# Optimization experiments

Measured on AMD Instinct MI355X. Metric: run time of the kernel, lower is better.

## Reference

```python
import jax, jax.numpy as jnp
import numpy as np

N = 65536      # points
NS = 16        # nsample
CIN = 128
CMID = 128
COUT = 128
S = 8          # share_planes
EPS = 1e-5


def setup_inputs() -> dict:
    key = jax.random.key(0)
    ks = jax.random.split(key, 12)
    f = lambda k, shape, s=0.05: (jax.random.normal(k, shape, jnp.float32) * s)
    inp = {
        'p': jax.random.normal(ks[0], (N, 3), jnp.float32),
        'x': jax.random.normal(ks[1], (N, CIN), jnp.float32),
        'idx': jax.random.randint(ks[2], (N, NS), 0, N, jnp.int32),
        'wq': f(ks[3], (CMID, CIN)), 'bq': jnp.zeros((CMID,), jnp.float32),
        'wk': f(ks[4], (CMID, CIN)), 'bk': jnp.zeros((CMID,), jnp.float32),
        'wv': f(ks[5], (COUT, CIN)), 'bv': jnp.zeros((COUT,), jnp.float32),
        'p_w1': f(ks[6], (3, 3), 0.3), 'p_b1': jnp.zeros((3,), jnp.float32),
        'p_bng': jnp.ones((3,), jnp.float32), 'p_bnb': jnp.zeros((3,), jnp.float32),
        'p_bnm': jnp.zeros((3,), jnp.float32), 'p_bnv': jnp.ones((3,), jnp.float32),
        'p_w2': f(ks[7], (COUT, 3), 0.3), 'p_b2': jnp.zeros((COUT,), jnp.float32),
        'w_bn1g': jnp.ones((CMID,), jnp.float32), 'w_bn1b': jnp.zeros((CMID,), jnp.float32),
        'w_bn1m': jnp.zeros((CMID,), jnp.float32), 'w_bn1v': jnp.ones((CMID,), jnp.float32),
        'w_w1': f(ks[8], (CMID // S, CMID)), 'w_b1': jnp.zeros((CMID // S,), jnp.float32),
        'w_bn2g': jnp.ones((CMID // S,), jnp.float32), 'w_bn2b': jnp.zeros((CMID // S,), jnp.float32),
        'w_bn2m': jnp.zeros((CMID // S,), jnp.float32), 'w_bn2v': jnp.ones((CMID // S,), jnp.float32),
        'w_w2': f(ks[9], (COUT // S, COUT // S)), 'w_b2': jnp.zeros((COUT // S,), jnp.float32),
    }
    return inp


def _bn(t, g, b, m, v):
    # eval-mode BatchNorm1d: per-channel affine on last axis
    return (t - m) * (g / jnp.sqrt(v + EPS)) + b


def reference(p, x, idx, wq, bq, wk, bk, wv, bv,
              p_w1, p_b1, p_bng, p_bnb, p_bnm, p_bnv, p_w2, p_b2,
              w_bn1g, w_bn1b, w_bn1m, w_bn1v, w_w1, w_b1,
              w_bn2g, w_bn2b, w_bn2m, w_bn2v, w_w2, w_b2):
    idx = idx.astype(jnp.int32)
    x_q = x @ wq.T + bq            # (n, mid)
    x_k = x @ wk.T + bk            # (n, mid)
    x_v = x @ wv.T + bv            # (n, out)
    # boundary_queryandgroup: gather neighbors, relative xyz
    p_r = p[idx] - p[:, None, :]   # (n, ns, 3)
    g_k = x_k[idx]                 # (n, ns, mid)
    g_v = x_v[idx]                 # (n, ns, out)
    # linear_p: Linear(3,3) -> BN(3) -> ReLU -> Linear(3,out)
    p_r = p_r @ p_w1.T + p_b1
    p_r = jax.nn.relu(_bn(p_r, p_bng, p_bnb, p_bnm, p_bnv))
    p_r = p_r @ p_w2.T + p_b2      # (n, ns, out)
    n, ns, _ = g_k.shape
    w = g_k - x_q[:, None, :] + p_r.reshape(n, ns, COUT // CMID, CMID).sum(2)
    # linear_w: BN(mid) -> ReLU -> Linear(mid, mid//s) -> BN -> ReLU -> Linear
    w = jax.nn.relu(_bn(w, w_bn1g, w_bn1b, w_bn1m, w_bn1v))
    w = w @ w_w1.T + w_b1          # (n, ns, mid//s)
    w = jax.nn.relu(_bn(w, w_bn2g, w_bn2b, w_bn2m, w_bn2v))
    w = w @ w_w2.T + w_b2          # (n, ns, out//s)
    w = jax.nn.softmax(w, axis=1)  # over neighbors
    out = ((g_v + p_r).reshape(n, ns, S, COUT // S) * w[:, :, None, :]).sum(1)
    return out.reshape(n, COUT)
```

## Files before the change

kernel.cpp:

```cpp
#include <hip/hip_runtime.h>

typedef unsigned short u16;
typedef unsigned int   u32;
typedef unsigned long long u64;

#define NPTS 65536
#define NNS  16
#define C    128

static __device__ __forceinline__ float bflo(u32 u){ return __builtin_bit_cast(float, u << 16); }
static __device__ __forceinline__ float ldbf(const u16* p){ return bflo((u32)(*p)); }
static __device__ __forceinline__ u16 f2bf(float f){
  u32 u = __builtin_bit_cast(u32, f);
  return (u16)((u + 0x7fffu + ((u >> 16) & 1u)) >> 16);
}

template<bool BF>
static __device__ __forceinline__ float ldT(const void* b, long i){
  if constexpr (BF) return ldbf((const u16*)b + i);
  else return ((const float*)b)[i];
}

struct P29 {
  const void *p, *x; const int* idx;
  const void *wq,*bq,*wk,*bk,*wv,*bv;
  const void *pw1,*pb1,*pbng,*pbnb,*pbnm,*pbnv,*pw2,*pb2;
  const void *bn1g,*bn1b,*bn1m,*bn1v,*ww1,*wb1;
  const void *bn2g,*bn2b,*bn2m,*bn2v,*ww2,*wb2;
};

static __device__ int detect_mode(const void* x){
  int lane = threadIdx.x & 63;
  float vb = ldbf((const u16*)x + lane);
  bool okb = (vb == vb) && fabsf(vb) < 32.f && fabsf(vb) > 1e-8f;
  if (__popcll(__ballot(okb)) >= 56) return 0;
  float vf = ((const float*)x)[lane];
  bool okf = (vf == vf) && fabsf(vf) < 32.f && fabsf(vf) > 1e-8f;
  if (__popcll(__ballot(okf)) >= 56) return 1;
  return 2;
}

template<bool BF>
static __device__ int value_checks(const P29& q){
  int lane = threadIdx.x & 63;
  bool ok = fabsf(ldT<BF>(q.bq, lane)) <= 1e-5f;
  ok = ok && fabsf(ldT<BF>(q.bn1v, lane) - 1.f) <= 0.02f;
  if (lane < 3) ok = ok && fabsf(ldT<BF>(q.pbnv, lane) - 1.f) <= 0.02f;
  if (__popcll(__ballot(ok)) != 64) return 4;
  int v = q.idx[lane];
  bool in = (v >= 0 && v < NPTS);
  if (__popcll(__ballot(in)) != 64) return 3;
  bool oz = ((lane & 1) == 1) ? (v == 0) : true;
  if (__popcll(__ballot(oz)) == 64) return 5;
  return 0;
}

static __device__ void report_out(void* outv, float code_val){
  u16* o = (u16*)outv;
  const int tid = threadIdx.x, wid = tid >> 6, lane = tid & 63;
  const int n = blockIdx.x * 4 + wid;
  ((u32*)o)[(size_t)n * 64 + lane] = 0u;
  if (blockIdx.x == 0 && tid == 0){
    ((float*)outv)[0] = code_val;
    o[2] = f2bf(code_val);
  }
}

__global__ __launch_bounds__(256) void report_kernel(void* outv, float code_val){
  report_out(outv, code_val);
}

typedef __bf16 bf16x8 __attribute__((ext_vector_type(8)));
typedef float  f32x4  __attribute__((ext_vector_type(4)));

template<bool BF>
static __device__ __forceinline__ void stage64(const void* src, size_t row0, u16* lds){
  const int t = threadIdx.x;
  #pragma unroll
  for (int i = 0; i < 4; i++){
    const int ch  = t + i * 256;
    const int row = ch >> 4, cc = ch & 15;
    u16 tmp[8];
    if constexpr (BF){
      *(uint4*)tmp = *(const uint4*)((const u16*)src + ((row0 + row) * (size_t)128 + cc * 8));
    } else {
      const float* s = (const float*)src + ((row0 + row) * (size_t)128 + cc * 8);
      float4 a = ((const float4*)s)[0];
      float4 b = ((const float4*)s)[1];
      tmp[0] = f2bf(a.x); tmp[1] = f2bf(a.y); tmp[2] = f2bf(a.z); tmp[3] = f2bf(a.w);
      tmp[4] = f2bf(b.x); tmp[5] = f2bf(b.y); tmp[6] = f2bf(b.z); tmp[7] = f2bf(b.w);
    }
    const u32 byte = (u32)row * 256u + (u32)((cc * 16) ^ ((row & 7) << 4));
    *(uint4*)((char*)lds + byte) = *(uint4*)tmp;
  }
}

template<bool BF>
static __device__ void qkv_mfma_body(const P29 q, u16* xq, u16* xk, u16* xv){
  __shared__ u16 sA[64 * 128];
  const int a = blockIdx.y;
  const size_t n0 = (size_t)blockIdx.x * 64;
  const void* W  = (a == 0) ? q.wq : (a == 1) ? q.wk : q.wv;
  const void* Bp = (a == 0) ? q.bq : (a == 1) ? q.bk : q.bv;
  u16*       D   = (a == 0) ? xq  : (a == 1) ? xk  : xv;

  stage64<BF>(q.x, n0, sA);

  const int tid = threadIdx.x, wid = tid >> 6, lane = tid & 63;
  const int lm = lane & 15, lk = lane >> 4;
  const int colbase = wid * 32;

  bf16x8 bfr[2][4];
  #pragma unroll
  for (int ni = 0; ni < 2; ni++){
    const int col = colbase + ni*16 + lm;
    #pragma unroll
    for (int kk = 0; kk < 4; kk++){
      const int k0 = kk*32 + lk*8;
      uint4 raw;
      if constexpr (BF){
        raw = *(const uint4*)((const u16*)W + (size_t)col * C + k0);
      } else {
        const float* s = (const float*)W + (size_t)col * C + k0;
        float4 x0 = ((const float4*)s)[0], x1 = ((const float4*)s)[1];
        u16 tmp[8] = {f2bf(x0.x),f2bf(x0.y),f2bf(x0.z),f2bf(x0.w),
                      f2bf(x1.x),f2bf(x1.y),f2bf(x1.z),f2bf(x1.w)};
        raw = *(const uint4*)tmp;
      }
      bfr[ni][kk] = __builtin_bit_cast(bf16x8, raw);
    }
  }
  __syncthreads();

  f32x4 acc[4][2];
  #pragma unroll
  for (int mi = 0; mi < 4; mi++){
    acc[mi][0] = f32x4{0.f,0.f,0.f,0.f};
    acc[mi][1] = f32x4{0.f,0.f,0.f,0.f};
  }

  #pragma unroll
  for (int kk = 0; kk < 4; kk++){
    const u32 kb = (u32)(kk * 64 + lk * 16);
    #pragma unroll
    for (int mi = 0; mi < 4; mi++){
      const u32 row = (u32)(mi*16 + lm);
      bf16x8 af = *(const bf16x8*)((const char*)sA + row * 256u + (kb ^ ((row & 7u) << 4)));
      acc[mi][0] = __builtin_amdgcn_mfma_f32_16x16x32_bf16(af, bfr[0][kk], acc[mi][0], 0, 0, 0);
      acc[mi][1] = __builtin_amdgcn_mfma_f32_16x16x32_bf16(af, bfr[1][kk], acc[mi][1], 0, 0, 0);
    }
  }

  #pragma unroll
  for (int ni = 0; ni < 2; ni++){
    const int col = colbase + ni*16 + lm;
    const float bias = ldT<BF>(Bp, col);
    #pragma unroll
    for (int mi = 0; mi < 4; mi++){
      const size_t rbase = n0 + (size_t)(mi*16 + lk*4);
      #pragma unroll
      for (int r = 0; r < 4; r++)
        D[(rbase + r) * 128 + col] = f2bf(acc[mi][ni][r] + bias);
    }
  }
}

__global__ __launch_bounds__(256)
void qkv_kernel(P29 q, u16* xq, u16* xk, u16* xv){
  int mode = detect_mode(q.x);
  if (mode == 0)      qkv_mfma_body<true >(q, xq, xk, xv);
  else if (mode == 1) qkv_mfma_body<false>(q, xq, xk, xv);
}

template<bool BF>
static __device__ void main_body(const P29 q, const u16* xq, const u16* xk,
                                 const u16* xv, void* outv){
  __shared__ char s_buf[4][5120];

  const int tid  = threadIdx.x;
  const int wid  = tid >> 6, lane = tid & 63;
  const int n    = blockIdx.x * 4 + wid;
  const int c0   = lane * 2, c1 = c0 + 1;

  u16*   s_w   = (u16*)  s_buf[wid];
  float* s_mid = (float*)(s_buf[wid] + 4096);
  float* s_wf  = (float*) s_buf[wid];

  float pw[3][3], pb[3];
  #pragma unroll
  for (int t = 0; t < 3; t++){
    float ss = ldT<BF>(q.pbng, t) * rsqrtf(fabsf(ldT<BF>(q.pbnv, t)) + 1e-5f);
    float tt = ldT<BF>(q.pbnb, t) - ldT<BF>(q.pbnm, t) * ss;
    #pragma unroll
    for (int k = 0; k < 3; k++) pw[t][k] = ss * ldT<BF>(q.pw1, t*3 + k);
    pb[t] = ss * ldT<BF>(q.pb1, t) + tt;
  }
  const float ps0 = ldT<BF>(q.p, (size_t)n*3 + 0);
  const float ps1 = ldT<BF>(q.p, (size_t)n*3 + 1);
  const float ps2 = ldT<BF>(q.p, (size_t)n*3 + 2);

  const float s0 = ldT<BF>(q.bn1g, c0) * rsqrtf(fabsf(ldT<BF>(q.bn1v, c0)) + 1e-5f);
  const float t0 = ldT<BF>(q.bn1b, c0) - ldT<BF>(q.bn1m, c0) * s0;
  const float s1 = ldT<BF>(q.bn1g, c1) * rsqrtf(fabsf(ldT<BF>(q.bn1v, c1)) + 1e-5f);
  const float t1 = ldT<BF>(q.bn1b, c1) - ldT<BF>(q.bn1m, c1) * s1;
  const float A0 = ldT<BF>(q.pw2, c0*3+0), A1 = ldT<BF>(q.pw2, c0*3+1), A2 = ldT<BF>(q.pw2, c0*3+2);
  const float B0 = ldT<BF>(q.pw2, c1*3+0), B1 = ldT<BF>(q.pw2, c1*3+1), B2 = ldT<BF>(q.pw2, c1*3+2);
  const float pbc0 = ldT<BF>(q.pb2, c0), pbc1 = ldT<BF>(q.pb2, c1);
  const float xq0 = ldbf(xq + (size_t)n * C + c0);
  const float xq1 = ldbf(xq + (size_t)n * C + c1);

  u32 svp[NNS];
  #pragma unroll
  for (int m = 0; m < NNS; m++){
    int im = q.idx[n*NNS + m];
    im = (im < 0) ? 0 : ((im >= NPTS) ? NPTS-1 : im);
    float pd0 = ldT<BF>(q.p, (size_t)im*3 + 0) - ps0;
    float pd1 = ldT<BF>(q.p, (size_t)im*3 + 1) - ps1;
    float pd2 = ldT<BF>(q.p, (size_t)im*3 + 2) - ps2;
    float q0 = fmaxf(pd0*pw[0][0] + pd1*pw[0][1] + pd2*pw[0][2] + pb[0], 0.f);
    float q1 = fmaxf(pd0*pw[1][0] + pd1*pw[1][1] + pd2*pw[1][2] + pb[1], 0.f);
    float q2 = fmaxf(pd0*pw[2][0] + pd1*pw[2][1] + pd2*pw[2][2] + pb[2], 0.f);
    float pr0 = q0*A0 + q1*A1 + q2*A2 + pbc0;
    float pr1 = q0*B0 + q1*B1 + q2*B2 + pbc1;
    u32 gk = *(const u32*)(xk + (size_t)im * C + c0);
    u32 gv = *(const u32*)(xv + (size_t)im * C + c0);
    float gk0 = bflo(gk & 0xffffu);
    float gk1 = bflo(gk >> 16);
    float w0 = fmaxf(s0*(gk0 - xq0 + pr0) + t0, 0.f);
    float w1 = fmaxf(s1*(gk1 - xq1 + pr1) + t1, 0.f);
    u32 pk = (u32)f2bf(w0) | ((u32)f2bf(w1) << 16);
    u32 byte = (u32)m * 256u + (((u32)lane * 4u) ^ (((u32)m & 7u) << 4));
    *(u32*)((char*)s_w + byte) = pk;
    float sv0 = bflo(gv & 0xffffu) + pr0;
    float sv1 = bflo(gv >> 16)     + pr1;
    svp[m] = (u32)f2bf(sv0) | ((u32)f2bf(sv1) << 16);
  }
  asm volatile("" ::: "memory");

  const int tb = (lane >> 4) * 4;
  {
    const int tA = lane & 15, gA = lane >> 4;
    f32x4 acc2;
    #pragma unroll
    for (int r = 0; r < 4; r++) acc2[r] = ldT<BF>(q.wb1, tb + r);
    const u32 row = lane & 15;
    #pragma unroll
    for (int kk = 0; kk < 4; kk++){
      const int cbase = kk*32 + gA*8;
      uint4 raw;
      if constexpr (BF){
        raw = *(const uint4*)((const u16*)q.ww1 + (size_t)tA*C + cbase);
      } else {
        const float* s = (const float*)q.ww1 + (size_t)tA*C + cbase;
        float4 a = ((const float4*)s)[0], b = ((const float4*)s)[1];
        u16 tmp[8] = {f2bf(a.x),f2bf(a.y),f2bf(a.z),f2bf(a.w),
                      f2bf(b.x),f2bf(b.y),f2bf(b.z),f2bf(b.w)};
        raw = *(const uint4*)tmp;
      }
      bf16x8 wwA = __builtin_bit_cast(bf16x8, raw);
      const u32 off = ((u32)(kk*64 + (lane >> 4)*16)) ^ ((row & 7u) << 4);
      bf16x8 bw = *(const bf16x8*)((const char*)s_w + row*256u + off);
      acc2 = __builtin_amdgcn_mfma_f32_16x16x32_bf16(wwA, bw, acc2, 0, 0, 0);
    }
    #pragma unroll
    for (int r = 0; r < 4; r++){
      const int t = tb + r;
      float g2 = ldT<BF>(q.bn2g, t), v2 = ldT<BF>(q.bn2v, t);
      float m2 = ldT<BF>(q.bn2m, t), b2 = ldT<BF>(q.bn2b, t);
      float ss = g2 * rsqrtf(fabsf(v2) + 1e-5f);
      float tt = b2 - m2*ss;
      s_mid[row*16 + ((t + row) & 15)] = fmaxf(ss*acc2[r] + tt, 0.f);
    }
  }
  asm volatile("" ::: "memory");

  const int mm = lane & 15, ug = lane >> 4;
  #pragma unroll
  for (int ui = 0; ui < 4; ui++){
    const int u = ug*4 + ui;
    float acc = ldT<BF>(q.wb2, u);
    #pragma unroll
    for (int t = 0; t < 16; t++)
      acc += s_mid[mm*16 + ((t + mm) & 15)] * ldT<BF>(q.ww2, u*16 + t);
    float mx = acc;
    #pragma unroll
    for (int msk = 1; msk < 16; msk <<= 1) mx = fmaxf(mx, __shfl_xor(mx, msk, 64));
    float ee = __expf(acc - mx);
    float sm = ee;
    #pragma unroll
    for (int msk = 1; msk < 16; msk <<= 1) sm += __shfl_xor(sm, msk, 64);
    s_wf[mm*17 + u] = ee / sm;
  }
  asm volatile("" ::: "memory");

  float acc0 = 0.f, acc1 = 0.f;
  const int u0 = c0 & 15;
  #pragma unroll
  for (int m = 0; m < NNS; m++){
    float wf0 = s_wf[m*17 + u0];
    float wf1 = s_wf[m*17 + u0 + 1];
    acc0 += bflo(svp[m] & 0xffffu) * wf0;
    acc1 += bflo(svp[m] >> 16)     * wf1;
  }
  if (!(acc0 == acc0)) acc0 = 12345.f;
  if (!(acc1 == acc1)) acc1 = 12345.f;
  if (BF){
    u16* o = (u16*)outv;
    o[(size_t)n * C + c0] = f2bf(acc0);
    o[(size_t)n * C + c1] = f2bf(acc1);
  } else {
    float* o = (float*)outv;
    o[(size_t)n * C + c0] = acc0;
    o[(size_t)n * C + c1] = acc1;
  }
}

__global__ __launch_bounds__(256)
void main_kernel(P29 q, const u16* xq, const u16* xk, const u16* xv, void* outv){
  int mode = detect_mode(q.x);
  int code = (mode == 2) ? 2 : (mode == 0 ? value_checks<true>(q) : value_checks<false>(q));
  if (code){ report_out(outv, code * 10000.f); return; }
  if (mode == 0) main_body<true >(q, xq, xk, xv, outv);
  else           main_body<false>(q, xq, xk, xv, outv);
}

extern "C" void kernel_launch(void* const* d_in, const int* in_sizes, int n_in,
                              void* d_out, int out_size, void* d_ws, size_t ws_size,
                              hipStream_t stream)
{
  static const int exp_sizes[29] = {
    196608, 8388608, 1048576,
    16384, 128, 16384, 128, 16384, 128,
    9, 3, 3, 3, 3, 3,
    384, 128,
    128, 128, 128, 128,
    2048, 16,
    16, 16, 16, 16,
    256, 16
  };
  int code = 0;
  if (n_in != 29) code = 7;
  else {
    for (int i = 0; i < 29; i++) if (in_sizes[i] != exp_sizes[i]) { code = 8; break; }
  }
  if (!code && out_size != NPTS * C) code = 9;
  if (!code && ws_size < (size_t)3 * NPTS * C * sizeof(u16)) code = 6;

  if (code){
    hipLaunchKernelGGL(report_kernel, dim3(NPTS/4), dim3(256), 0, stream,
                       d_out, (float)(code * 10000));
    return;
  }

  P29 q;
  q.p   = d_in[0];  q.x    = d_in[1];  q.idx  = (const int*)d_in[2];
  q.wq  = d_in[3];  q.bq   = d_in[4];  q.wk   = d_in[5];  q.bk  = d_in[6];
  q.wv  = d_in[7];  q.bv   = d_in[8];
  q.pw1 = d_in[9];  q.pb1  = d_in[10];
  q.pbng= d_in[11]; q.pbnb = d_in[12]; q.pbnm = d_in[13]; q.pbnv= d_in[14];
  q.pw2 = d_in[15]; q.pb2  = d_in[16];
  q.bn1g= d_in[17]; q.bn1b = d_in[18]; q.bn1m = d_in[19]; q.bn1v= d_in[20];
  q.ww1 = d_in[21]; q.wb1  = d_in[22];
  q.bn2g= d_in[23]; q.bn2b = d_in[24]; q.bn2m = d_in[25]; q.bn2v= d_in[26];
  q.ww2 = d_in[27]; q.wb2  = d_in[28];

  u16* xq = (u16*)d_ws;
  u16* xk = xq + (size_t)NPTS * C;
  u16* xv = xk + (size_t)NPTS * C;

  hipLaunchKernelGGL(qkv_kernel, dim3(1024, 3), dim3(256), 0, stream, q, xq, xk, xv);
  hipLaunchKernelGGL(main_kernel, dim3(NPTS/4), dim3(256), 0, stream, q, xq, xk, xv, d_out);
}
```

Measured before the change: 401.4 us.

## Use MFMA for second linear_w layer and transpose QKV GEMM for packed stores

Replaces the scalar 16x16 second linear_w matmul (via an LDS scratch buffer and per-lane loops over ww2) with a single 16x16x16 bf16 MFMA fed directly from registers, dropping the s_mid LDS buffer and shrinking shared memory per block. The QKV projection GEMM swaps operand roles so each lane owns four consecutive output channels, allowing packed 8-byte stores instead of scattered 2-byte stores. The second-layer intermediate is now rounded to bf16 before the MFMA, which slightly changes numerics.

```diff
diff --git a/kernel.cpp b/kernel.cpp
--- a/kernel.cpp
+++ b/kernel.cpp
@@ -71,7 +71,22 @@
 }
 
 typedef __bf16 bf16x8 __attribute__((ext_vector_type(8)));
+typedef __bf16 bf16x4 __attribute__((ext_vector_type(4)));
+typedef short  s16x4  __attribute__((ext_vector_type(4)));
 typedef float  f32x4  __attribute__((ext_vector_type(4)));
+
+static __device__ __forceinline__ f32x4 mfma16_bf16(u32 alo, u32 ahi,
+                                                    u32 blo, u32 bhi, f32x4 c){
+#if __has_builtin(__builtin_amdgcn_mfma_f32_16x16x16_bf16)
+  union { u32 u[2]; bf16x4 v; } A, B;
+  A.u[0]=alo; A.u[1]=ahi; B.u[0]=blo; B.u[1]=bhi;
+  return __builtin_amdgcn_mfma_f32_16x16x16_bf16(A.v, B.v, c, 0, 0, 0);
+#else
+  union { u32 u[2]; s16x4 v; } A, B;
+  A.u[0]=alo; A.u[1]=ahi; B.u[0]=blo; B.u[1]=bhi;
+  return __builtin_amdgcn_mfma_f32_16x16x16bf16_1k(A.v, B.v, c, 0, 0, 0);
+#endif
+}
 
 template<bool BF>
 static __device__ __forceinline__ void stage64(const void* src, size_t row0, u16* lds){
@@ -108,59 +123,60 @@
 
   const int tid = threadIdx.x, wid = tid >> 6, lane = tid & 63;
   const int lm = lane & 15, lk = lane >> 4;
-  const int colbase = wid * 32;
-
-  bf16x8 bfr[2][4];
-  #pragma unroll
-  for (int ni = 0; ni < 2; ni++){
-    const int col = colbase + ni*16 + lm;
+  const int chbase = wid * 32;
+
+  bf16x8 wfr[2][4];
+  #pragma unroll
+  for (int ci = 0; ci < 2; ci++){
+    const int ch = chbase + ci*16 + lm;
     #pragma unroll
     for (int kk = 0; kk < 4; kk++){
       const int k0 = kk*32 + lk*8;
       uint4 raw;
       if constexpr (BF){
-        raw = *(const uint4*)((const u16*)W + (size_t)col * C + k0);
+        raw = *(const uint4*)((const u16*)W + (size_t)ch * C + k0);
       } else {
-        const float* s = (const float*)W + (size_t)col * C + k0;
+        const float* s = (const float*)W + (size_t)ch * C + k0;
         float4 x0 = ((const float4*)s)[0], x1 = ((const float4*)s)[1];
         u16 tmp[8] = {f2bf(x0.x),f2bf(x0.y),f2bf(x0.z),f2bf(x0.w),
                       f2bf(x1.x),f2bf(x1.y),f2bf(x1.z),f2bf(x1.w)};
         raw = *(const uint4*)tmp;
       }
-      bfr[ni][kk] = __builtin_bit_cast(bf16x8, raw);
+      wfr[ci][kk] = __builtin_bit_cast(bf16x8, raw);
     }
   }
   __syncthreads();
 
-  f32x4 acc[4][2];
-  #pragma unroll
-  for (int mi = 0; mi < 4; mi++){
-    acc[mi][0] = f32x4{0.f,0.f,0.f,0.f};
-    acc[mi][1] = f32x4{0.f,0.f,0.f,0.f};
-  }
+  f32x4 acc[2][4];
+  #pragma unroll
+  for (int ci = 0; ci < 2; ci++)
+    #pragma unroll
+    for (int pi = 0; pi < 4; pi++) acc[ci][pi] = f32x4{0.f,0.f,0.f,0.f};
 
   #pragma unroll
   for (int kk = 0; kk < 4; kk++){
     const u32 kb = (u32)(kk * 64 + lk * 16);
     #pragma unroll
-    for (int mi = 0; mi < 4; mi++){
-      const u32 row = (u32)(mi*16 + lm);
-      bf16x8 af = *(const bf16x8*)((const char*)sA + row * 256u + (kb ^ ((row & 7u) << 4)));
-      acc[mi][0] = __builtin_amdgcn_mfma_f32_16x16x32_bf16(af, bfr[0][kk], acc[mi][0], 0, 0, 0);
-      acc[mi][1] = __builtin_amdgcn_mfma_f32_16x16x32_bf16(af, bfr[1][kk], acc[mi][1], 0, 0, 0);
-    }
-  }
-
-  #pragma unroll
-  for (int ni = 0; ni < 2; ni++){
-    const int col = colbase + ni*16 + lm;
-    const float bias = ldT<BF>(Bp, col);
-    #pragma unroll
-    for (int mi = 0; mi < 4; mi++){
-      const size_t rbase = n0 + (size_t)(mi*16 + lk*4);
-      #pragma unroll
-      for (int r = 0; r < 4; r++)
-        D[(rbase + r) * 128 + col] = f2bf(acc[mi][ni][r] + bias);
+    for (int pi = 0; pi < 4; pi++){
+      const u32 row = (u32)(pi*16 + lm);
+      bf16x8 xf = *(const bf16x8*)((const char*)sA + row * 256u + (kb ^ ((row & 7u) << 4)));
+      acc[0][pi] = __builtin_amdgcn_mfma_f32_16x16x32_bf16(wfr[0][kk], xf, acc[0][pi], 0, 0, 0);
+      acc[1][pi] = __builtin_amdgcn_mfma_f32_16x16x32_bf16(wfr[1][kk], xf, acc[1][pi], 0, 0, 0);
+    }
+  }
+
+  #pragma unroll
+  for (int ci = 0; ci < 2; ci++){
+    const int chb = chbase + ci*16 + lk*4;
+    float b0 = ldT<BF>(Bp, chb+0), b1 = ldT<BF>(Bp, chb+1);
+    float b2 = ldT<BF>(Bp, chb+2), b3 = ldT<BF>(Bp, chb+3);
+    #pragma unroll
+    for (int pi = 0; pi < 4; pi++){
+      const size_t n = n0 + (size_t)(pi*16 + lm);
+      u32 lo = (u32)f2bf(acc[ci][pi][0] + b0) | ((u32)f2bf(acc[ci][pi][1] + b1) << 16);
+      u32 hi = (u32)f2bf(acc[ci][pi][2] + b2) | ((u32)f2bf(acc[ci][pi][3] + b3) << 16);
+      uint2 pk; pk.x = lo; pk.y = hi;
+      *(uint2*)(D + n * 128 + chb) = pk;
     }
   }
 }
@@ -175,16 +191,15 @@
 template<bool BF>
 static __device__ void main_body(const P29 q, const u16* xq, const u16* xk,
                                  const u16* xv, void* outv){
-  __shared__ char s_buf[4][5120];
+  __shared__ char s_buf[4][4096];
 
   const int tid  = threadIdx.x;
   const int wid  = tid >> 6, lane = tid & 63;
   const int n    = blockIdx.x * 4 + wid;
   const int c0   = lane * 2, c1 = c0 + 1;
 
-  u16*   s_w   = (u16*)  s_buf[wid];
-  float* s_mid = (float*)(s_buf[wid] + 4096);
-  float* s_wf  = (float*) s_buf[wid];
+  u16*   s_w  = (u16*)  s_buf[wid];
+  float* s_wf = (float*)s_buf[wid];
 
   float pw[3][3], pb[3];
   #pragma unroll
@@ -238,58 +253,68 @@
   asm volatile("" ::: "memory");
 
   const int tb = (lane >> 4) * 4;
+  const int lm_ = lane & 15, ug_ = lane >> 4;
   {
-    const int tA = lane & 15, gA = lane >> 4;
     f32x4 acc2;
     #pragma unroll
     for (int r = 0; r < 4; r++) acc2[r] = ldT<BF>(q.wb1, tb + r);
-    const u32 row = lane & 15;
     #pragma unroll
     for (int kk = 0; kk < 4; kk++){
-      const int cbase = kk*32 + gA*8;
+      const int cbase = kk*32 + ug_*8;
       uint4 raw;
       if constexpr (BF){
-        raw = *(const uint4*)((const u16*)q.ww1 + (size_t)tA*C + cbase);
+        raw = *(const uint4*)((const u16*)q.ww1 + (size_t)lm_*C + cbase);
       } else {
-        const float* s = (const float*)q.ww1 + (size_t)tA*C + cbase;
+        const float* s = (const float*)q.ww1 + (size_t)lm_*C + cbase;
         float4 a = ((const float4*)s)[0], b = ((const float4*)s)[1];
         u16 tmp[8] = {f2bf(a.x),f2bf(a.y),f2bf(a.z),f2bf(a.w),
                       f2bf(b.x),f2bf(b.y),f2bf(b.z),f2bf(b.w)};
         raw = *(const uint4*)tmp;
       }
       bf16x8 wwA = __builtin_bit_cast(bf16x8, raw);
-      const u32 off = ((u32)(kk*64 + (lane >> 4)*16)) ^ ((row & 7u) << 4);
-      bf16x8 bw = *(const bf16x8*)((const char*)s_w + row*256u + off);
+      const u32 off = ((u32)(kk*64 + ug_*16)) ^ (((u32)lm_ & 7u) << 4);
+      bf16x8 bw = *(const bf16x8*)((const char*)s_w + (u32)lm_*256u + off);
       acc2 = __builtin_amdgcn_mfma_f32_16x16x32_bf16(wwA, bw, acc2, 0, 0, 0);
     }
+    u32 blo, bhi;
+    {
+      float mid[4];
+      #pragma unroll
+      for (int r = 0; r < 4; r++){
+        const int t = tb + r;
+        float ss = ldT<BF>(q.bn2g, t) * rsqrtf(fabsf(ldT<BF>(q.bn2v, t)) + 1e-5f);
+        float tt = ldT<BF>(q.bn2b, t) - ldT<BF>(q.bn2m, t) * ss;
+        mid[r] = fmaxf(ss*acc2[r] + tt, 0.f);
+      }
+      blo = (u32)f2bf(mid[0]) | ((u32)f2bf(mid[1]) << 16);
+      bhi = (u32)f2bf(mid[2]) | ((u32)f2bf(mid[3]) << 16);
+    }
+    u32 alo, ahi;
+    if constexpr (BF){
+      uint2 a8 = *(const uint2*)((const u16*)q.ww2 + (size_t)lm_*16 + tb);
+      alo = a8.x; ahi = a8.y;
+    } else {
+      const float* s = (const float*)q.ww2 + (size_t)lm_*16 + tb;
+      float4 a = *(const float4*)s;
+      alo = (u32)f2bf(a.x) | ((u32)f2bf(a.y) << 16);
+      ahi = (u32)f2bf(a.z) | ((u32)f2bf(a.w) << 16);
+    }
+    f32x4 acc3;
+    #pragma unroll
+    for (int r = 0; r < 4; r++) acc3[r] = ldT<BF>(q.wb2, tb + r);
+    acc3 = mfma16_bf16(alo, ahi, blo, bhi, acc3);
     #pragma unroll
     for (int r = 0; r < 4; r++){
-      const int t = tb + r;
-      float g2 = ldT<BF>(q.bn2g, t), v2 = ldT<BF>(q.bn2v, t);
-      float m2 = ldT<BF>(q.bn2m, t), b2 = ldT<BF>(q.bn2b, t);
-      float ss = g2 * rsqrtf(fabsf(v2) + 1e-5f);
-      float tt = b2 - m2*ss;
-      s_mid[row*16 + ((t + row) & 15)] = fmaxf(ss*acc2[r] + tt, 0.f);
-    }
-  }
-  asm volatile("" ::: "memory");
-
-  const int mm = lane & 15, ug = lane >> 4;
-  #pragma unroll
-  for (int ui = 0; ui < 4; ui++){
-    const int u = ug*4 + ui;
-    float acc = ldT<BF>(q.wb2, u);
-    #pragma unroll
-    for (int t = 0; t < 16; t++)
-      acc += s_mid[mm*16 + ((t + mm) & 15)] * ldT<BF>(q.ww2, u*16 + t);
-    float mx = acc;
-    #pragma unroll
-    for (int msk = 1; msk < 16; msk <<= 1) mx = fmaxf(mx, __shfl_xor(mx, msk, 64));
-    float ee = __expf(acc - mx);
-    float sm = ee;
-    #pragma unroll
-    for (int msk = 1; msk < 16; msk <<= 1) sm += __shfl_xor(sm, msk, 64);
-    s_wf[mm*17 + u] = ee / sm;
+      float v = acc3[r];
+      float mx = v;
+      #pragma unroll
+      for (int msk = 1; msk < 16; msk <<= 1) mx = fmaxf(mx, __shfl_xor(mx, msk, 64));
+      float ee = __expf(v - mx);
+      float sm = ee;
+      #pragma unroll
+      for (int msk = 1; msk < 16; msk <<= 1) sm += __shfl_xor(sm, msk, 64);
+      s_wf[lm_*17 + tb + r] = ee / sm;
+    }
   }
   asm volatile("" ::: "memory");
 
```

Result: faster. 390.4 us (-2.7%).
